# Performance work log

Measured on AMD Instinct MI355X. Metric: run time of the kernel, lower is better.

The kernel has to match this reference:

```python
import jax, jax.numpy as jnp
import numpy as np

B, S, E = 8, 4096, 128

def _prelu(x, a):
    return jnp.where(x >= 0, x, a * x)

def setup_inputs() -> dict:
    key = jax.random.key(0)
    ks = jax.random.split(key, 7)
    lim = 1.0 / np.sqrt(E)
    x = jax.random.normal(ks[0], (B, S, E), dtype=jnp.float32)
    Wq = jax.random.uniform(ks[1], (E, E), jnp.float32, -lim, lim)
    Wk = jax.random.uniform(ks[2], (E, E), jnp.float32, -lim, lim)
    Wv = jax.random.uniform(ks[3], (E, E), jnp.float32, -lim, lim)
    bq = jax.random.uniform(ks[4], (E,), jnp.float32, -lim, lim)
    bk = jax.random.uniform(ks[5], (E,), jnp.float32, -lim, lim)
    bv = jax.random.uniform(ks[6], (E,), jnp.float32, -lim, lim)
    # PReLU default: single shared slope initialized to 0.25
    aq = jnp.array(0.25, dtype=jnp.float32)
    ak = jnp.array(0.25, dtype=jnp.float32)
    av = jnp.array(0.25, dtype=jnp.float32)
    return {"x": x, "Wq": Wq, "bq": bq, "aq": aq,
            "Wk": Wk, "bk": bk, "ak": ak,
            "Wv": Wv, "bv": bv, "av": av}

def reference(x, Wq, bq, aq, Wk, bk, ak, Wv, bv, av):
    # Linear (y = x @ W.T + b) followed by PReLU, per nn.Sequential(Linear, PReLU)
    qx = _prelu(jnp.einsum('bse,fe->bsf', x, Wq) + bq, aq)  # [B,S,E]
    kx = _prelu(jnp.einsum('bse,fe->bsf', x, Wk) + bk, ak)
    vx = _prelu(jnp.einsum('bse,fe->bsf', x, Wv) + bv, av)
    scale = 1.0 / jnp.sqrt(jnp.asarray(E, dtype=x.dtype))
    qk = jnp.einsum('bqe,bke->bqk', qx, kx) * scale  # [B,S,S]
    attn = jax.nn.softmax(qk, axis=2)
    return jnp.einsum('bqk,bke->bqe', attn, vx)  # [B,S,E]
```

## Files before the change

kernel.cpp:

```cpp
#include <hip/hip_runtime.h>
#include <hip/hip_bf16.h>
#include <stdint.h>

typedef __bf16 bf16x8 __attribute__((ext_vector_type(8)));
typedef float f32x4 __attribute__((ext_vector_type(4)));
typedef float f32x16 __attribute__((ext_vector_type(16)));
typedef unsigned int u32x4 __attribute__((ext_vector_type(4)));

static constexpr int Bn = 8, Sn = 4096, En = 128;

__device__ __forceinline__ unsigned short f2bf(float f) {
  unsigned u = __builtin_bit_cast(unsigned, f);
  u += 0x7fffu + ((u >> 16) & 1u);
  return (unsigned short)(u >> 16);
}

__device__ __forceinline__ float bf2f(unsigned short s) {
  return __builtin_bit_cast(float, (unsigned)s << 16);
}

__device__ __forceinline__ unsigned cvtpk(float a, float b) {
  unsigned r;
  asm("v_cvt_pk_bf16_f32 %0, %1, %2" : "=v"(r) : "v"(a), "v"(b));
  return r;
}

__device__ __forceinline__ void plswap(unsigned &a, unsigned &b) {
  asm("v_permlane32_swap_b32 %0, %1" : "+v"(a), "+v"(b));
}

__global__ __launch_bounds__(256) void qkv_kernel(
    const float* __restrict__ x,
    const float* __restrict__ Wq, const float* __restrict__ bq, const float* __restrict__ aq,
    const float* __restrict__ Wk, const float* __restrict__ bk, const float* __restrict__ ak,
    const float* __restrict__ Wv, const float* __restrict__ bv, const float* __restrict__ av,
    unsigned short* __restrict__ qo, unsigned short* __restrict__ kf,
    unsigned short* __restrict__ vf)
{
  __shared__ __align__(16) unsigned short xs[64 * 136];
  __shared__ __align__(16) unsigned short wsh[128 * 136];
  const int tid = threadIdx.x;
  const int r0 = blockIdx.x * 64;

  for (int i = 0; i < 8; ++i) {
    int cid = tid + i * 256;
    int row = cid >> 5, c4 = cid & 31;
    const float4 v = *(const float4*)&x[(size_t)(r0 + row) * 128 + c4 * 4];
    unsigned short* d = &xs[row * 136 + c4 * 4];
    d[0] = f2bf(v.x); d[1] = f2bf(v.y); d[2] = f2bf(v.z); d[3] = f2bf(v.w);
  }

  const int lane = tid & 63, wid = tid >> 6;
  const int g = lane >> 4, ln = lane & 15;
  const float* Ws[3] = {Wq, Wk, Wv};
  const float* Bs[3] = {bq, bk, bv};
  const float* As[3] = {aq, ak, av};
  bf16x8 afrag[4];

  for (int mat = 0; mat < 3; ++mat) {
    __syncthreads();
    for (int i = 0; i < 16; ++i) {
      int cid = tid + i * 256;
      int row = cid >> 5, c4 = cid & 31;
      const float4 v = *(const float4*)&Ws[mat][row * 128 + c4 * 4];
      unsigned short* d = &wsh[row * 136 + c4 * 4];
      d[0] = f2bf(v.x); d[1] = f2bf(v.y); d[2] = f2bf(v.z); d[3] = f2bf(v.w);
    }
    __syncthreads();

    if (mat == 0) {
      for (int ks = 0; ks < 4; ++ks)
        afrag[ks] = *(const bf16x8*)&xs[(wid * 16 + ln) * 136 + ks * 32 + g * 8];
    }
    const float alpha = As[mat][0];
    f32x4 acc[8];
    for (int nt = 0; nt < 8; ++nt) acc[nt] = (f32x4)(0.f);
    for (int nt = 0; nt < 8; ++nt)
      for (int ks = 0; ks < 4; ++ks) {
        bf16x8 bfrag = *(const bf16x8*)&wsh[(nt * 16 + ln) * 136 + ks * 32 + g * 8];
        acc[nt] = __builtin_amdgcn_mfma_f32_16x16x32_bf16(afrag[ks], bfrag, acc[nt], 0, 0, 0);
      }
    const int mbase = r0 + wid * 16 + g * 4;
    for (int nt = 0; nt < 8; ++nt) {
      const int n = nt * 16 + ln;
      const float bias = Bs[mat][n];
      float vv[4];
      for (int r = 0; r < 4; ++r) {
        float t = acc[nt][r] + bias;
        vv[r] = t >= 0.f ? t : alpha * t;
      }
      if (mat == 0) {
        for (int r = 0; r < 4; ++r) qo[(size_t)(mbase + r) * 128 + n] = f2bf(vv[r]);
      } else if (mat == 1) {
        for (int r = 0; r < 4; ++r) {
          const int key = mbase + r, bb = key >> 12, sl = key & 4095;
          const size_t addr = ((size_t)bb << 20) + (size_t)(sl >> 5) * 8192
                            + nt * 1024 + ((ln >> 3) & 1) * 512
                            + (sl & 31) * 16 + ((ln & 7) << 1);
          *(unsigned short*)((char*)kf + addr) = f2bf(vv[r]);
        }
      } else {
        const int bb = mbase >> 12, sl = mbase & 4095;
        const int kb64 = sl >> 6, kk = sl & 63;
        const int ks2 = kk >> 4, hi2 = (kk >> 3) & 1, j0 = kk & 7;
        const size_t addr = ((size_t)bb << 20) + (size_t)kb64 * 16384
                          + (n >> 5) * 4096 + ks2 * 1024 + hi2 * 512
                          + (n & 31) * 16 + (j0 << 1);
        ushort4 pk;
        pk.x = f2bf(vv[0]); pk.y = f2bf(vv[1]); pk.z = f2bf(vv[2]); pk.w = f2bf(vv[3]);
        *(ushort4*)((char*)vf + addr) = pk;
      }
    }
  }
}

__device__ __forceinline__ void load_frag(const char* kfb, const char* vfb, int kt,
                                          int tid, uint4* kr, uint4* vr) {
  const char* ks = kfb + (size_t)kt * 16384;
  const char* vs = vfb + (size_t)kt * 16384;
  kr[0] = *(const uint4*)(ks + tid * 16);
  kr[1] = *(const uint4*)(ks + 8192 + tid * 16);
  vr[0] = *(const uint4*)(vs + tid * 16);
  vr[1] = *(const uint4*)(vs + 8192 + tid * 16);
}

__device__ __forceinline__ void store_frag(char* slot, int tid,
                                           const uint4* kr, const uint4* vr) {
  *(uint4*)(slot + tid * 16) = kr[0];
  *(uint4*)(slot + 8192 + tid * 16) = kr[1];
  *(uint4*)(slot + 16384 + tid * 16) = vr[0];
  *(uint4*)(slot + 24576 + tid * 16) = vr[1];
}

template <int KSPLIT>
__global__ __launch_bounds__(512, 2) void attn_kernel(
    const unsigned short* __restrict__ q,
    const unsigned short* __restrict__ kf,
    const unsigned short* __restrict__ vf,
    unsigned short* __restrict__ opart, float* __restrict__ mpart,
    float* __restrict__ lpart, float* __restrict__ out)
{
  __shared__ __align__(16) char smem[98304];
  const int tid = threadIdx.x;
  const int lane = tid & 63, wid = tid >> 6;
  const int NS = 8 * KSPLIT;
  const int bid = blockIdx.x;
  const int s_ = bid % NS;
  const int qt = bid / NS;
  const int b  = s_ / KSPLIT;
  const int kh = s_ % KSPLIT;
  const int hi = lane >> 5, ln = lane & 31;
  const size_t bOff = (size_t)b * Sn * En;

  const int nkt = (Sn / KSPLIT) / 64;
  const int kbase = kh * (Sn / KSPLIT);
  const char* kfb = (const char*)kf + ((size_t)b << 20) + (size_t)(kbase >> 5) * 8192;
  const char* vfb = (const char*)vf + ((size_t)b << 20) + (size_t)(kbase >> 6) * 16384;

  const int qrow = qt * 256 + wid * 32 + ln;
  bf16x8 qf[8];
  #pragma unroll
  for (int s = 0; s < 8; ++s)
    qf[s] = *(const bf16x8*)((const char*)(q + bOff) + (size_t)qrow * 256 + s * 32 + hi * 16);

  f32x16 acc[4];
  #pragma unroll
  for (int et = 0; et < 4; ++et) acc[et] = (f32x16)(0.f);
  float m_run = -1e30f, lsum = 0.f;

  const float cst = 1.4426950408889634f * 0.08838834764831845f;

  auto qk = [&](const char* slot, f32x16& st0, f32x16& st1) {
    const char* kp = slot + hi * 512 + ln * 16;
    st0 = (f32x16)(0.f); st1 = (f32x16)(0.f);
    __builtin_amdgcn_s_setprio(1);
    #pragma unroll
    for (int s = 0; s < 8; ++s) {
      bf16x8 kf0 = *(const bf16x8*)(kp + s * 1024);
      bf16x8 kf1 = *(const bf16x8*)(kp + 8192 + s * 1024);
      st0 = __builtin_amdgcn_mfma_f32_32x32x16_bf16(kf0, qf[s], st0, 0, 0, 0);
      st1 = __builtin_amdgcn_mfma_f32_32x32x16_bf16(kf1, qf[s], st1, 0, 0, 0);
    }
    __builtin_amdgcn_s_setprio(0);
  };

  auto sm_pv = [&](const char* slot, const f32x16& st0, const f32x16& st1) {
    const char* vp = slot + 16384 + hi * 512 + ln * 16;
    float t16[16];
    #pragma unroll
    for (int i = 0; i < 16; ++i) t16[i] = fmaxf(st0[i], st1[i]);
    float t8[8];
    #pragma unroll
    for (int i = 0; i < 8; ++i) t8[i] = fmaxf(t16[i], t16[i + 8]);
    float t4[4];
    #pragma unroll
    for (int i = 0; i < 4; ++i) t4[i] = fmaxf(t8[i], t8[i + 4]);
    float vtile = fmaxf(fmaxf(t4[0], t4[1]), fmaxf(t4[2], t4[3])) * cst;
    vtile = fmaxf(vtile, __shfl_xor(vtile, 32));

    if (__any(vtile > m_run + 8.0f)) {
      float mnew = fmaxf(m_run, vtile);
      float al = __builtin_amdgcn_exp2f(m_run - mnew);
      #pragma unroll
      for (int et = 0; et < 4; ++et) acc[et] *= al;
      lsum *= al;
      m_run = mnew;
    }

    float p[32];
    #pragma unroll
    for (int i = 0; i < 16; ++i) p[i]      = __builtin_amdgcn_exp2f(fmaf(st0[i], cst, -m_run));
    #pragma unroll
    for (int i = 0; i < 16; ++i) p[16 + i] = __builtin_amdgcn_exp2f(fmaf(st1[i], cst, -m_run));

    float s16[16];
    #pragma unroll
    for (int i = 0; i < 16; ++i) s16[i] = p[i] + p[16 + i];
    float s8[8];
    #pragma unroll
    for (int i = 0; i < 8; ++i) s8[i] = s16[i] + s16[i + 8];
    float s4[4];
    #pragma unroll
    for (int i = 0; i < 4; ++i) s4[i] = s8[i] + s8[i + 4];
    float tsum = (s4[0] + s4[1]) + (s4[2] + s4[3]);
    tsum += __shfl_xor(tsum, 32);
    lsum += tsum;

    unsigned wa[8], wb[8];
    #pragma unroll
    for (int g2 = 0; g2 < 8; ++g2) {
      wa[g2] = cvtpk(p[4 * g2], p[4 * g2 + 1]);
      wb[g2] = cvtpk(p[4 * g2 + 2], p[4 * g2 + 3]);
    }
    bf16x8 pb[4];
    #pragma unroll
    for (int ks = 0; ks < 4; ++ks) {
      unsigned w0 = wa[2 * ks], w2 = wa[2 * ks + 1];
      plswap(w0, w2);
      unsigned w1 = wb[2 * ks], w3 = wb[2 * ks + 1];
      plswap(w1, w3);
      u32x4 w = {w0, w1, w2, w3};
      pb[ks] = __builtin_bit_cast(bf16x8, w);
    }

    __builtin_amdgcn_s_setprio(1);
    #pragma unroll
    for (int ks = 0; ks < 4; ++ks) {
      #pragma unroll
      for (int et = 0; et < 4; ++et) {
        bf16x8 vfr = *(const bf16x8*)(vp + et * 4096 + ks * 1024);
        acc[et] = __builtin_amdgcn_mfma_f32_32x32x16_bf16(vfr, pb[ks], acc[et], 0, 0, 0);
      }
    }
    __builtin_amdgcn_s_setprio(0);
  };

  char* s0 = smem;
  char* s1 = smem + 32768;
  char* s2 = smem + 65536;

  uint4 kregA[2], vregA[2], kregB[2], vregB[2];
  load_frag(kfb, vfb, 0, tid, kregA, vregA);
  store_frag(s0, tid, kregA, vregA);
  load_frag(kfb, vfb, 1, tid, kregB, vregB);
  store_frag(s1, tid, kregB, vregB);
  if (nkt > 2) load_frag(kfb, vfb, 2, tid, kregA, vregA);
  __syncthreads();
  f32x16 sA0, sA1, sB0, sB1;
  qk(s0, sA0, sA1);

  for (int t = 0; t < nkt; t += 2) {
    if (t + 2 < nkt) store_frag(s2, tid, kregA, vregA);
    if (t + 3 < nkt) load_frag(kfb, vfb, t + 3, tid, kregB, vregB);
    qk(s1, sB0, sB1);
    sm_pv(s0, sA0, sA1);
    __syncthreads();

    if (t + 3 < nkt) store_frag(s0, tid, kregB, vregB);
    if (t + 4 < nkt) load_frag(kfb, vfb, t + 4, tid, kregA, vregA);
    if (t + 2 < nkt) qk(s2, sA0, sA1);
    sm_pv(s1, sB0, sB1);
    __syncthreads();

    char* tt = s0; s0 = s2; s2 = s1; s1 = tt;
  }

  if (KSPLIT > 1 && lane < 32) {
    const size_t idx = (size_t)kh * (Bn * Sn) + (size_t)b * Sn + qt * 256 + wid * 32 + ln;
    mpart[idx] = m_run;
    lpart[idx] = lsum;
  }

  __syncthreads();
  const float inv = (KSPLIT == 1) ? (1.0f / lsum) : 1.0f;
  char* sl = smem + wid * 8192;
  char* outb;
  if (KSPLIT == 1)
    outb = (char*)(out + ((size_t)b * Sn + qt * 256 + wid * 32) * En);
  else
    outb = (char*)(opart + ((size_t)kh * (Bn * Sn) + (size_t)b * Sn + qt * 256 + wid * 32) * En);

  #pragma unroll
  for (int h = 0; h < 2; ++h) {
    #pragma unroll
    for (int e2 = 0; e2 < 2; ++e2) {
      const int et = 2 * h + e2;
      #pragma unroll
      for (int rg = 0; rg < 4; ++rg) {
        f32x4 v;
        #pragma unroll
        for (int j = 0; j < 4; ++j) v[j] = acc[et][rg * 4 + j] * inv;
        const int addr = ln * 256 + e2 * 128 + rg * 32 + hi * 16;
        *(f32x4*)(sl + (addr ^ ((ln & 7) << 4))) = v;
      }
    }
    asm volatile("s_waitcnt lgkmcnt(0)" ::: "memory");
    __builtin_amdgcn_sched_barrier(0);
    #pragma unroll
    for (int i = 0; i < 8; ++i) {
      const int flat = i * 1024 + lane * 16;
      const int qr = flat >> 8, col = flat & 255;
      f32x4 v = *(const f32x4*)(sl + ((qr * 256 + col) ^ ((qr & 7) << 4)));
      if (KSPLIT == 1) {
        *(f32x4*)(outb + (size_t)qr * 512 + h * 256 + col) = v;
      } else {
        ushort4 pk;
        pk.x = f2bf(v[0]); pk.y = f2bf(v[1]); pk.z = f2bf(v[2]); pk.w = f2bf(v[3]);
        *(ushort4*)(outb + (size_t)qr * 256 + h * 128 + (col >> 1)) = pk;
      }
    }
    if (h == 0) {
      asm volatile("s_waitcnt lgkmcnt(0)" ::: "memory");
      __builtin_amdgcn_sched_barrier(0);
    }
  }
}

template <int NSPLIT>
__global__ __launch_bounds__(256) void combine_kernel(
    const unsigned short* __restrict__ op, const float* __restrict__ mp,
    const float* __restrict__ lp, float* __restrict__ out)
{
  const int idx = blockIdx.x * 256 + threadIdx.x;
  const int row = idx >> 5;
  const int BS = Bn * Sn;
  float m = -1e30f;
  #pragma unroll
  for (int j = 0; j < NSPLIT; ++j) m = fmaxf(m, mp[j * BS + row]);
  float den = 0.f;
  f32x4 sum = (f32x4)(0.f);
  #pragma unroll
  for (int j = 0; j < NSPLIT; ++j) {
    const float w = __builtin_amdgcn_exp2f(mp[j * BS + row] - m);
    den += w * lp[j * BS + row];
    ushort4 u = *(const ushort4*)(op + (size_t)j * ((size_t)BS * En) + (size_t)idx * 4);
    f32x4 o;
    o[0] = bf2f(u.x); o[1] = bf2f(u.y); o[2] = bf2f(u.z); o[3] = bf2f(u.w);
    sum += o * w;
  }
  const float inv = 1.f / den;
  ((f32x4*)out)[idx] = sum * inv;
}

extern "C" void kernel_launch(void* const* d_in, const int* in_sizes, int n_in,
                              void* d_out, int out_size, void* d_ws, size_t ws_size,
                              hipStream_t stream) {
  const float* x  = (const float*)d_in[0];
  const float* Wq = (const float*)d_in[1];
  const float* bq = (const float*)d_in[2];
  const float* aq = (const float*)d_in[3];
  const float* Wk = (const float*)d_in[4];
  const float* bk = (const float*)d_in[5];
  const float* ak = (const float*)d_in[6];
  const float* Wv = (const float*)d_in[7];
  const float* bv = (const float*)d_in[8];
  const float* av = (const float*)d_in[9];

  const size_t BSE = (size_t)Bn * Sn * En;
  const size_t BS  = (size_t)Bn * Sn;
  char* base = (char*)d_ws;
  unsigned short* qws = (unsigned short*)base;
  unsigned short* kws = qws + BSE;
  unsigned short* vws = kws + BSE;
  const size_t fixed = 3 * BSE * 2;
  unsigned short* opart = (unsigned short*)(base + fixed);

  auto need = [&](int j) { return fixed + (size_t)j * BSE * 2 + (size_t)j * BS * 8; };
  int split = 1;
  if (ws_size >= need(2)) split = 2;

  float* mpart = (float*)(base + fixed + (size_t)split * BSE * 2);
  float* lpart = mpart + (size_t)split * BS;

  qkv_kernel<<<512, 256, 0, stream>>>(x, Wq, bq, aq, Wk, bk, ak, Wv, bv, av,
                                      qws, kws, vws);
  if (split == 2) {
    attn_kernel<2><<<256, 512, 0, stream>>>(qws, kws, vws, opart, mpart, lpart,
                                            (float*)d_out);
    combine_kernel<2><<<4096, 256, 0, stream>>>(opart, mpart, lpart, (float*)d_out);
  } else {
    attn_kernel<1><<<128, 512, 0, stream>>>(qws, kws, vws, opart, mpart, lpart,
                                            (float*)d_out);
  }
}
```

Before: 139.7 us.

## Pre-convert QKV weights to bf16 once and double rows per projection block

Adds a small kernel that converts Wq/Wk/Wv to bf16 into workspace once, so the projection kernel copies bf16 weight tiles with 16-byte loads instead of re-reading and converting fp32 weights in every block. The projection kernel now handles 128 rows per block with 512 threads, which halves the number of weight tile loads across the grid. In exchange it adds an extra kernel launch, uses more shared memory per block, and needs extra workspace that is now counted in the split check.

```diff
diff --git a/kernel.cpp b/kernel.cpp
--- a/kernel.cpp
+++ b/kernel.cpp
@@ -29,21 +29,34 @@
   asm("v_permlane32_swap_b32 %0, %1" : "+v"(a), "+v"(b));
 }
 
-__global__ __launch_bounds__(256) void qkv_kernel(
-    const float* __restrict__ x,
-    const float* __restrict__ Wq, const float* __restrict__ bq, const float* __restrict__ aq,
-    const float* __restrict__ Wk, const float* __restrict__ bk, const float* __restrict__ ak,
-    const float* __restrict__ Wv, const float* __restrict__ bv, const float* __restrict__ av,
+__global__ __launch_bounds__(256) void wconv_kernel(
+    const float* __restrict__ Wq, const float* __restrict__ Wk,
+    const float* __restrict__ Wv, unsigned short* __restrict__ wb)
+{
+  const int f4 = blockIdx.x * 256 + threadIdx.x;
+  const int mat = f4 >> 12, off = f4 & 4095;
+  const float* src = (mat == 0) ? Wq : (mat == 1) ? Wk : Wv;
+  const float4 v = *(const float4*)&src[off * 4];
+  ushort4 pk;
+  pk.x = f2bf(v.x); pk.y = f2bf(v.y); pk.z = f2bf(v.z); pk.w = f2bf(v.w);
+  *(ushort4*)&wb[(size_t)mat * 16384 + off * 4] = pk;
+}
+
+__global__ __launch_bounds__(512) void qkv_kernel(
+    const float* __restrict__ x, const unsigned short* __restrict__ wb,
+    const float* __restrict__ bq, const float* __restrict__ aq,
+    const float* __restrict__ bk, const float* __restrict__ ak,
+    const float* __restrict__ bv, const float* __restrict__ av,
     unsigned short* __restrict__ qo, unsigned short* __restrict__ kf,
     unsigned short* __restrict__ vf)
 {
-  __shared__ __align__(16) unsigned short xs[64 * 136];
+  __shared__ __align__(16) unsigned short xs[128 * 136];
   __shared__ __align__(16) unsigned short wsh[128 * 136];
   const int tid = threadIdx.x;
-  const int r0 = blockIdx.x * 64;
+  const int r0 = blockIdx.x * 128;
 
   for (int i = 0; i < 8; ++i) {
-    int cid = tid + i * 256;
+    int cid = tid + i * 512;
     int row = cid >> 5, c4 = cid & 31;
     const float4 v = *(const float4*)&x[(size_t)(r0 + row) * 128 + c4 * 4];
     unsigned short* d = &xs[row * 136 + c4 * 4];
@@ -52,19 +65,17 @@
 
   const int lane = tid & 63, wid = tid >> 6;
   const int g = lane >> 4, ln = lane & 15;
-  const float* Ws[3] = {Wq, Wk, Wv};
   const float* Bs[3] = {bq, bk, bv};
   const float* As[3] = {aq, ak, av};
   bf16x8 afrag[4];
 
   for (int mat = 0; mat < 3; ++mat) {
     __syncthreads();
-    for (int i = 0; i < 16; ++i) {
-      int cid = tid + i * 256;
-      int row = cid >> 5, c4 = cid & 31;
-      const float4 v = *(const float4*)&Ws[mat][row * 128 + c4 * 4];
-      unsigned short* d = &wsh[row * 136 + c4 * 4];
-      d[0] = f2bf(v.x); d[1] = f2bf(v.y); d[2] = f2bf(v.z); d[3] = f2bf(v.w);
+    for (int i = 0; i < 4; ++i) {
+      int cid = tid + i * 512;
+      int row = cid >> 4, c8 = cid & 15;
+      *(uint4*)&wsh[row * 136 + c8 * 8] =
+          *(const uint4*)&wb[(size_t)mat * 16384 + row * 128 + c8 * 8];
     }
     __syncthreads();
 
@@ -226,18 +237,18 @@
     tsum += __shfl_xor(tsum, 32);
     lsum += tsum;
 
-    unsigned wa[8], wb[8];
+    unsigned wa[8], wb2[8];
     #pragma unroll
     for (int g2 = 0; g2 < 8; ++g2) {
-      wa[g2] = cvtpk(p[4 * g2], p[4 * g2 + 1]);
-      wb[g2] = cvtpk(p[4 * g2 + 2], p[4 * g2 + 3]);
+      wa[g2]  = cvtpk(p[4 * g2], p[4 * g2 + 1]);
+      wb2[g2] = cvtpk(p[4 * g2 + 2], p[4 * g2 + 3]);
     }
     bf16x8 pb[4];
     #pragma unroll
     for (int ks = 0; ks < 4; ++ks) {
       unsigned w0 = wa[2 * ks], w2 = wa[2 * ks + 1];
       plswap(w0, w2);
-      unsigned w1 = wb[2 * ks], w3 = wb[2 * ks + 1];
+      unsigned w1 = wb2[2 * ks], w3 = wb2[2 * ks + 1];
       plswap(w1, w3);
       u32x4 w = {w0, w1, w2, w3};
       pb[ks] = __builtin_bit_cast(bf16x8, w);
@@ -385,14 +396,18 @@
   const size_t fixed = 3 * BSE * 2;
   unsigned short* opart = (unsigned short*)(base + fixed);
 
-  auto need = [&](int j) { return fixed + (size_t)j * BSE * 2 + (size_t)j * BS * 8; };
+  auto need = [&](int j) {
+    return fixed + (size_t)j * BSE * 2 + (size_t)j * BS * 8 + 98304;
+  };
   int split = 1;
   if (ws_size >= need(2)) split = 2;
 
   float* mpart = (float*)(base + fixed + (size_t)split * BSE * 2);
   float* lpart = mpart + (size_t)split * BS;
-
-  qkv_kernel<<<512, 256, 0, stream>>>(x, Wq, bq, aq, Wk, bk, ak, Wv, bv, av,
+  unsigned short* wb = (unsigned short*)(lpart + (size_t)split * BS);
+
+  wconv_kernel<<<48, 256, 0, stream>>>(Wq, Wk, Wv, wb);
+  qkv_kernel<<<256, 512, 0, stream>>>(x, wb, bq, aq, bk, ak, bv, av,
                                       qws, kws, vws);
   if (split == 2) {
     attn_kernel<2><<<256, 512, 0, stream>>>(qws, kws, vws, opart, mpart, lpart,
```

After: 134.8 us (median of 2 runs). 3.5% less time.
